# Optimization experiments

Measured on AMD Instinct MI355X. Metric: run time of the kernel, lower is better.

Reference implementation:

```python
import jax, jax.numpy as jnp
import numpy as np

N_NODES = 10000
N_EDGES = 320000
MUL = 32            # multiplicity of each irrep block (32x0e + 32x1o)
H = 4               # attention heads (divides MUL)
D_IN = MUL + 3 * MUL  # 128
N_BASIS = 8         # radial basis size (edge_scalar_attr dim)
HID = 64            # features=[64] hidden layer of the weight-MLP
INV3 = 1.0 / np.sqrt(3.0)  # CG normalization for 1o x 1o -> 0e


def _mlp(x, w1, b1, w2):
    # HTensorProductMLP weight net: edge scalars -> per-path uvu weights
    h = jax.nn.gelu(x @ w1 * (1.0 / np.sqrt(N_BASIS)) + b1)
    return (h @ w2) * (1.0 / np.sqrt(HID))  # (E, 4*MUL)


def _tp_uvu(w, xs, xv, ys, yv):
    # uvu tensor product of (32x0e+32x1o) x (1x0e+1x1o) keeping {0e,1o} outputs.
    # Sorted output blocks: [0e: s*s, 0e: v.v, 1o: s*v, 1o: v*s]
    w = w.reshape(-1, 4, MUL)
    o0 = w[:, 0] * xs * ys[:, None]                              # (E,MUL)
    o1 = w[:, 1] * jnp.einsum('eud,ed->eu', xv, yv) * INV3       # (E,MUL)
    o2 = w[:, 2][:, :, None] * xs[:, :, None] * yv[:, None, :]   # (E,MUL,3)
    o3 = w[:, 3][:, :, None] * xv * ys[:, None, None]            # (E,MUL,3)
    return o0, o1, o2, o3


def setup_inputs() -> dict:
    key = jax.random.key(0)
    ks = jax.random.split(key, 13)
    E, N = N_EDGES, N_NODES
    return {
        'edge_src': jax.random.randint(ks[0], (E,), 0, N, dtype=jnp.int32),
        'edge_dst': jax.random.randint(ks[1], (E,), 0, N, dtype=jnp.int32),
        'edge_scalar_attr': jax.random.uniform(ks[2], (E, N_BASIS), dtype=jnp.float32),
        'edge_attr': jax.random.normal(ks[3], (E, 4), dtype=jnp.float32),
        'edge_weight_cutoff': jax.random.uniform(ks[4], (E,), dtype=jnp.float32),
        'node_f': jax.random.normal(ks[5], (N, D_IN), dtype=jnp.float32),
        'wk1': jax.random.normal(ks[6], (N_BASIS, HID), dtype=jnp.float32),
        'bk1': jnp.zeros((HID,), jnp.float32),
        'wk2': jax.random.normal(ks[7], (HID, 4 * MUL), dtype=jnp.float32),
        'wv1': jax.random.normal(ks[8], (N_BASIS, HID), dtype=jnp.float32),
        'bv1': jnp.zeros((HID,), jnp.float32),
        'wv2': jax.random.normal(ks[9], (HID, 4 * MUL), dtype=jnp.float32),
        'W_dot': jax.random.normal(ks[10], (4, H, MUL, MUL), dtype=jnp.float32),
        'W_lin_s': jax.random.normal(ks[11], (2 * MUL, MUL), dtype=jnp.float32),
        'W_lin_v': jax.random.normal(ks[12], (2 * MUL, MUL), dtype=jnp.float32),
    }


def reference(edge_src, edge_dst, edge_scalar_attr, edge_attr, edge_weight_cutoff,
              node_f, wk1, bk1, wk2, wv1, bv1, wv2, W_dot, W_lin_s, W_lin_v):
    N = node_f.shape[0]
    xs = node_f[:, :MUL]                       # (N,MUL)   0e block
    xv = node_f[:, MUL:].reshape(N, MUL, 3)    # (N,MUL,3) 1o block
    ys = edge_attr[:, 0]                       # (E,)  Y_0
    yv = edge_attr[:, 1:4]                     # (E,3) Y_1
    sxs, sxv = xs[edge_src], xv[edge_src]      # gather source node feats

    # keys: per-edge equivariant tensor-product MLP
    wk = _mlp(edge_scalar_attr, wk1, bk1, wk2)
    k0, k1, kv0, kv1 = _tp_uvu(wk, sxs, sxv, ys, yv)

    # attention logits: fully-connected TP (dst node, key) -> Hx0e
    qs, qv = xs[edge_dst], xv[edge_dst]
    inv_fan = 1.0 / np.sqrt(4.0 * MUL * MUL)
    d = (jnp.einsum('huv,eu,ev->eh', W_dot[0], qs, k0)
         + jnp.einsum('huv,eu,ev->eh', W_dot[1], qs, k1)
         + jnp.einsum('huv,eud,evd->eh', W_dot[2], qv, kv0) * INV3
         + jnp.einsum('huv,eud,evd->eh', W_dot[3], qv, kv1) * INV3) * inv_fan
    expw = edge_weight_cutoff[:, None] * jnp.exp(d)              # (E,H)
    z = jax.ops.segment_sum(expw, edge_dst, num_segments=N)      # (N,H)
    z = jnp.where(z == 0.0, 1.0, z)
    alpha = expw / z[edge_dst]                                   # (E,H)

    # values: second per-edge equivariant tensor-product MLP
    wv = _mlp(edge_scalar_attr, wv1, bv1, wv2)
    v0, v1, vv0, vv1 = _tp_uvu(wv, sxs, sxv, ys, yv)
    sa = jnp.sqrt(jax.nn.relu(alpha))                            # (E,H)
    Ee = sa.shape[0]
    m = MUL // H
    e0 = (v0.reshape(Ee, H, m) * sa[:, :, None]).reshape(Ee, MUL)
    e1 = (v1.reshape(Ee, H, m) * sa[:, :, None]).reshape(Ee, MUL)
    e2 = (vv0.reshape(Ee, H, m, 3) * sa[:, :, None, None]).reshape(Ee, 3 * MUL)
    e3 = (vv1.reshape(Ee, H, m, 3) * sa[:, :, None, None]).reshape(Ee, 3 * MUL)
    edge_v = jnp.concatenate([e0, e1, e2, e3], axis=-1)          # (E, 8*MUL)

    agg = jax.ops.segment_sum(edge_v, edge_dst, num_segments=N)  # (N, 8*MUL)

    # equivariant HLinear: mix multiplicities within each irrep
    s = agg[:, :2 * MUL]                                         # (N,2*MUL)
    v = agg[:, 2 * MUL:].reshape(N, 2 * MUL, 3)                  # (N,2*MUL,3)
    inv_l = 1.0 / np.sqrt(2.0 * MUL)
    out_s = (s @ W_lin_s) * inv_l                                # (N,MUL)
    out_v = jnp.einsum('nud,uw->nwd', v, W_lin_v) * inv_l        # (N,MUL,3)
    return jnp.concatenate([out_s, out_v.reshape(N, 3 * MUL)], axis=-1)
```

## Files before the change

kernel.cpp:

```cpp
#include <hip/hip_runtime.h>


constexpr float INV3    = 0.57735026918962576f;
constexpr float INV_SQ8 = 0.35355339059327373f;
constexpr float INV_HID = 0.125f;
constexpr float INV_FAN = 0.015625f;
constexpr float INV_L   = 0.125f;
constexpr int   MAXD    = 128;

__device__ __forceinline__ float gelu_tanh(float x) {
  float u = 0.7978845608028654f * (x + 0.044715f * x * x * x);
  float e = __expf(2.0f * u);
  return x * (1.0f - 1.0f / (e + 1.0f));
}

__global__ void k_zero(int* __restrict__ p, int n) {
  int i = blockIdx.x * 256 + threadIdx.x;
  if (i < n) p[i] = 0;
}

__global__ void k_hist(const int* __restrict__ dst, int* __restrict__ cnt, int E) {
  int e = blockIdx.x * 256 + threadIdx.x;
  if (e < E) atomicAdd(&cnt[dst[e]], 1);
}

__global__ __launch_bounds__(256) void k_scan(const int* __restrict__ cnt,
                                              int* __restrict__ rowptr, int N) {
  __shared__ int wsum[4];
  __shared__ int woff[4];
  __shared__ int carry;
  int t = threadIdx.x, wave = t >> 6, lane = t & 63;
  if (t == 0) { carry = 0; rowptr[0] = 0; }
  __syncthreads();
  for (int base = 0; base < N; base += 256) {
    int i = base + t;
    int inc = (i < N) ? cnt[i] : 0;
#pragma unroll
    for (int off = 1; off < 64; off <<= 1) {
      int y = __shfl_up(inc, off, 64);
      if (lane >= off) inc += y;
    }
    if (lane == 63) wsum[wave] = inc;
    __syncthreads();
    if (t == 0) {
      int r = 0;
      for (int w = 0; w < 4; w++) { woff[w] = r; r += wsum[w]; }
    }
    __syncthreads();
    int incl = inc + woff[wave] + carry;
    if (i < N) rowptr[i + 1] = incl;
    __syncthreads();
    if (t == 255) carry = incl;
    __syncthreads();
  }
}

__global__ void k_fill(const int* __restrict__ dst, const int* __restrict__ rowptr,
                       int* __restrict__ cursor, int* __restrict__ csr, int E) {
  int e = blockIdx.x * 256 + threadIdx.x;
  if (e < E) {
    int d = dst[e];
    int s = atomicAdd(&cursor[d], 1);
    csr[rowptr[d] + s] = e;
  }
}

__global__ void k_dhist(const int* __restrict__ rowptr, int* __restrict__ dbin, int N) {
  int n = blockIdx.x * 256 + threadIdx.x;
  if (n < N) {
    int deg = rowptr[n + 1] - rowptr[n];
    atomicAdd(&dbin[min(deg, 127)], 1);
  }
}

__global__ void k_dscan(const int* __restrict__ dbin, int* __restrict__ doff) {
  if (threadIdx.x == 0 && blockIdx.x == 0) {
    int r = 0;
    for (int d = 127; d >= 0; --d) { doff[d] = r; r += dbin[d]; }
  }
}

__global__ void k_dfill(const int* __restrict__ rowptr, const int* __restrict__ doff,
                        int* __restrict__ dcur, int* __restrict__ nperm, int N) {
  int n = blockIdx.x * 256 + threadIdx.x;
  if (n < N) {
    int d = min(rowptr[n + 1] - rowptr[n], 127);
    int p = doff[d] + atomicAdd(&dcur[d], 1);
    nperm[p] = n;
  }
}

__global__ __launch_bounds__(256) void k_gather(
    const int* __restrict__ csr, const int* __restrict__ esrc,
    const float* __restrict__ xattr, const float* __restrict__ eattr,
    const float* __restrict__ cutoff,
    float* __restrict__ xc, float* __restrict__ ec, float* __restrict__ cc,
    int* __restrict__ srcc, int E) {
  int p = blockIdx.x * 256 + threadIdx.x;
  if (p >= E) return;
  int e = csr[p];
  srcc[p] = esrc[e];
  cc[p] = cutoff[e];
  ((float4*)ec)[p] = ((const float4*)eattr)[e];
  const float4* xs = (const float4*)xattr + (size_t)e * 2;
  float4* xd = (float4*)xc + (size_t)p * 2;
  xd[0] = xs[0]; xd[1] = xs[1];
}

__global__ __launch_bounds__(256) void k_nodeA(const float* __restrict__ node_f,
                                               const float* __restrict__ Wdot,
                                               float* __restrict__ A, int N) {
  __shared__ float Wd[16384];
  __shared__ float nfs[32 * 128];
  int t = threadIdx.x;
  for (int i = t; i < 16384; i += 256) Wd[i] = Wdot[i];
  int n0 = blockIdx.x * 32;
  int nEnd = min(32, N - n0);
  for (int i = t; i < nEnd * 128; i += 256) nfs[i] = node_f[n0 * 128 + i];
  __syncthreads();
  for (int nn = 0; nn < nEnd; ++nn) {
    const float* nf = &nfs[nn * 128];
    float* An = &A[(n0 + nn) * 1024];
#pragma unroll
    for (int k = 0; k < 4; k++) {
      int o = t + k * 256;
      float acc = 0.f;
      int idx;
      if (o < 256) {
        int term = o >> 7, h = (o >> 5) & 3, v = o & 31;
        const float* W = &Wd[term * 4096 + h * 1024 + v];
#pragma unroll
        for (int u = 0; u < 32; u++) acc += W[u * 32] * nf[u];
        idx = term * 128 + v * 4 + h;
      } else {
        int r = o - 256;
        int term = r / 384;
        int rr = r % 384;
        int h = rr / 96, q = rr % 96, v = q / 3, d = q - 3 * (q / 3);
        const float* W = &Wd[(term + 2) * 4096 + h * 1024 + v];
#pragma unroll
        for (int u = 0; u < 32; u++) acc += W[u * 32] * nf[32 + u * 3 + d];
        idx = 256 + term * 384 + v * 12 + h * 3 + d;
      }
      An[idx] = acc;
    }
  }
}

__global__ __launch_bounds__(256) void k_mlp(
    const float* __restrict__ xc,
    const float* __restrict__ w1, const float* __restrict__ b1,
    const float* __restrict__ w2,
    float* __restrict__ wm,
    int E, int chunk)
{
  __shared__ __align__(16) float w1s[512];
  __shared__ float b1s[64];
  __shared__ __align__(16) float wq[16][128][4];
  __shared__ __align__(16) float Hs[4][4][64];

  int t = threadIdx.x;
  int wave = t >> 6, lane = t & 63;
  for (int i = t; i < 512; i += 256) w1s[i] = w1[i];
  if (t < 64) b1s[t] = b1[t];
  for (int i = t; i < 8192; i += 256) { int l = i >> 7, j = i & 127; wq[l >> 2][j][l & 3] = w2[i]; }
  __syncthreads();

  int base = blockIdx.x * chunk;
  int end = min(base + chunk, E);
  int v = lane & 31;
  bool hi = lane >= 32;

  for (int sb = base + wave * 4; sb < end; sb += 16) {
    int sl[4];
#pragma unroll
    for (int k = 0; k < 4; k++) sl[k] = min(sb + k, E - 1);
    float h[4];
#pragma unroll
    for (int k = 0; k < 4; k++) {
      const float4* xp = (const float4*)xc + (size_t)sl[k] * 2;
      float4 xa = xp[0], xb = xp[1];
      float acc = xa.x * w1s[lane]       + xa.y * w1s[64 + lane]
                + xa.z * w1s[128 + lane] + xa.w * w1s[192 + lane]
                + xb.x * w1s[256 + lane] + xb.y * w1s[320 + lane]
                + xb.z * w1s[384 + lane] + xb.w * w1s[448 + lane];
      h[k] = gelu_tanh(acc * INV_SQ8 + b1s[lane]);
    }
#pragma unroll
    for (int k = 0; k < 4; k++) Hs[wave][k][lane] = h[k];
    float a0[4] = {0, 0, 0, 0}, a1[4] = {0, 0, 0, 0};
#pragma unroll
    for (int q = 0; q < 16; q++) {
      float4 wA = *(const float4*)&wq[q][lane][0];
      float4 wB = *(const float4*)&wq[q][lane + 64][0];
#pragma unroll
      for (int k = 0; k < 4; k++) {
        float4 hq = *(const float4*)&Hs[wave][k][q * 4];
        a0[k] += hq.x * wA.x + hq.y * wA.y + hq.z * wA.z + hq.w * wA.w;
        a1[k] += hq.x * wB.x + hq.y * wB.y + hq.z * wB.z + hq.w * wB.w;
      }
    }
#pragma unroll
    for (int k = 0; k < 4; k++) {
      if (sb + k < end) {
        float2 o = make_float2(a0[k] * INV_HID, a1[k] * INV_HID);
        ((float2*)wm)[(size_t)sl[k] * 64 + (hi ? 32 : 0) + v] = o;
      }
    }
  }
}

__global__ __launch_bounds__(256) void k_att(
    const int* __restrict__ rowptr,
    const int* __restrict__ nperm,
    const int* __restrict__ srcc,
    const float* __restrict__ ec,
    const float* __restrict__ cc,
    const float* __restrict__ node_f,
    const float* __restrict__ wm,
    const float* __restrict__ A,
    float* __restrict__ sa_out,
    int N)
{
  __shared__ float expws[4][MAXD][4];

  int t = threadIdx.x;
  int wave = t >> 6, lane = t & 63;
  int idx = blockIdx.x * 4 + wave;
  if (idx >= N) return;
  int n = nperm[idx];
  int row0 = rowptr[n];
  int deg = min(rowptr[n + 1] - row0, MAXD);
  if (deg <= 0) return;

  int v = lane & 31;
  bool hi = lane >= 32;
  int kk = (lane >> 2) & 3;

  float aS[4], aV[12];
  {
    const float* Ab = A + (size_t)n * 1024;
    const float* ps = Ab + (hi ? 128 : 0) + v * 4;
    float4 t0 = *(const float4*)ps;
    aS[0] = t0.x; aS[1] = t0.y; aS[2] = t0.z; aS[3] = t0.w;
    const float* pv = Ab + (hi ? 640 : 256) + v * 12;
    float4 u0 = *(const float4*)pv;
    float4 u1 = *(const float4*)(pv + 4);
    float4 u2 = *(const float4*)(pv + 8);
    aV[0] = u0.x; aV[1] = u0.y; aV[2]  = u0.z; aV[3]  = u0.w;
    aV[4] = u1.x; aV[5] = u1.y; aV[6]  = u1.z; aV[7]  = u1.w;
    aV[8] = u2.x; aV[9] = u2.y; aV[10] = u2.z; aV[11] = u2.w;
  }

  int iters = (deg + 3) >> 2;
  float zacc = 0.f;

  for (int it = 0; it < iters; ++it) {
    int sb = it * 4;
    int slot[4]; int sp[4];
#pragma unroll
    for (int k = 0; k < 4; k++) slot[k] = row0 + min(sb + k, deg - 1);
#pragma unroll
    for (int k = 0; k < 4; k++) sp[k] = srcc[slot[k]];
    float4 ya[4]; float cf[4]; float2 wj[4]; float s0[4], s1[4], s2[4];
#pragma unroll
    for (int k = 0; k < 4; k++) {
      ya[k] = ((const float4*)ec)[slot[k]];
      cf[k] = (sb + k < deg) ? cc[slot[k]] : 0.f;
      wj[k] = ((const float2*)wm)[(size_t)slot[k] * 64 + (hi ? 32 : 0) + v];
      const float* nf = &node_f[(size_t)sp[k] * 128];
      if (!hi) { s0[k] = nf[v]; s1[k] = 0.f; s2[k] = 0.f; }
      else     { s0[k] = nf[32 + v * 3]; s1[k] = nf[33 + v * 3]; s2[k] = nf[34 + v * 3]; }
    }
    float p[16];
#pragma unroll
    for (int k = 0; k < 4; k++) {
      float ys = ya[k].x, yv0 = ya[k].y, yv1 = ya[k].z, yv2 = ya[k].w;
      if (!hi) {
        float k0 = wj[k].x * s0[k] * ys;
        float kb = INV3 * wj[k].y * s0[k];
#pragma unroll
        for (int h2 = 0; h2 < 4; h2++)
          p[k * 4 + h2] = aS[h2] * k0 +
              kb * (aV[h2 * 3] * yv0 + aV[h2 * 3 + 1] * yv1 + aV[h2 * 3 + 2] * yv2);
      } else {
        float dotv = s0[k] * yv0 + s1[k] * yv1 + s2[k] * yv2;
        float k1 = wj[k].x * dotv * INV3;
        float kc = INV3 * wj[k].y * ys;
#pragma unroll
        for (int h2 = 0; h2 < 4; h2++)
          p[k * 4 + h2] = aS[h2] * k1 +
              kc * (aV[h2 * 3] * s0[k] + aV[h2 * 3 + 1] * s1[k] + aV[h2 * 3 + 2] * s2[k]);
      }
    }
    bool fb0 = (lane & 1) != 0;
    float q8[8];
#pragma unroll
    for (int j = 0; j < 8; j++) {
      float a = p[2 * j], b = p[2 * j + 1];
      float keep = fb0 ? b : a, send = fb0 ? a : b;
      q8[j] = keep + __shfl_xor(send, 1, 64);
    }
    bool fb1 = (lane & 2) != 0;
    float r4[4];
#pragma unroll
    for (int j = 0; j < 4; j++) {
      float a = q8[2 * j], b = q8[2 * j + 1];
      float keep = fb1 ? b : a, send = fb1 ? a : b;
      r4[j] = keep + __shfl_xor(send, 2, 64);
    }
    bool fb2 = (lane & 4) != 0;
    float s2v[2];
#pragma unroll
    for (int j = 0; j < 2; j++) {
      float a = r4[2 * j], b = r4[2 * j + 1];
      float keep = fb2 ? b : a, send = fb2 ? a : b;
      s2v[j] = keep + __shfl_xor(send, 4, 64);
    }
    bool fb3 = (lane & 8) != 0;
    float w;
    {
      float a = s2v[0], b = s2v[1];
      float keep = fb3 ? b : a, send = fb3 ? a : b;
      w = keep + __shfl_xor(send, 8, 64);
    }
    w += __shfl_xor(w, 16, 64);
    w += __shfl_xor(w, 32, 64);
    float cA = (lane & 4) ? cf[1] : cf[0];
    float cB = (lane & 4) ? cf[3] : cf[2];
    float cfs = (lane & 8) ? cB : cA;
    int slotw = sb + kk;
    float ex = cfs * __expf(w * INV_FAN);
    if (lane < 16 && slotw < deg) {
      expws[wave][slotw][lane & 3] = ex;
      zacc += ex;
    }
  }
  float zr = zacc;
  zr += __shfl_xor(zr, 4, 64);
  zr += __shfl_xor(zr, 8, 64);
  float zf = __shfl(zr, lane & 3, 64);
  zf = (zf == 0.f) ? 1.f : zf;
  for (int i = lane; i < deg * 4; i += 64) {
    int slot = i >> 2;
    float alpha = expws[wave][slot][lane & 3] / zf;
    sa_out[(size_t)(row0 + slot) * 4 + (lane & 3)] = sqrtf(fmaxf(alpha, 0.f));
  }
}

__global__ __launch_bounds__(256) void k_agg(
    const int* __restrict__ rowptr,
    const int* __restrict__ nperm,
    const int* __restrict__ srcc,
    const float* __restrict__ ec,
    const float* __restrict__ node_f,
    const float* __restrict__ wm,
    const float* __restrict__ Wls, const float* __restrict__ Wlv,
    const float* __restrict__ sa_in,
    float* __restrict__ out,
    int N)
{
  __shared__ float aggv[4][256];

  int t = threadIdx.x;
  int wave = t >> 6, lane = t & 63;
  int idx = blockIdx.x * 4 + wave;
  if (idx >= N) return;
  int n = nperm[idx];
  int row0 = rowptr[n];
  int deg = min(rowptr[n + 1] - row0, MAXD);

  int v = lane & 31;
  bool hi = lane >= 32;
  int hh = v >> 3;
  float accS = 0.f, acc0 = 0.f, acc1 = 0.f, acc2 = 0.f;

  if (deg > 0) {
    int iters = (deg + 3) >> 2;
    for (int it = 0; it < iters; ++it) {
      int sb = it * 4;
      int slot[4]; int sp[4];
#pragma unroll
      for (int k = 0; k < 4; k++) slot[k] = row0 + min(sb + k, deg - 1);
#pragma unroll
      for (int k = 0; k < 4; k++) sp[k] = srcc[slot[k]];
      float4 ya[4]; float sav[4]; float2 wj[4]; float s0[4], s1[4], s2[4];
#pragma unroll
      for (int k = 0; k < 4; k++) {
        sav[k] = (sb + k < deg) ? sa_in[(size_t)slot[k] * 4 + hh] : 0.f;
        ya[k] = ((const float4*)ec)[slot[k]];
        wj[k] = ((const float2*)wm)[(size_t)slot[k] * 64 + (hi ? 32 : 0) + v];
        const float* nf = &node_f[(size_t)sp[k] * 128];
        if (!hi) { s0[k] = nf[v]; s1[k] = 0.f; s2[k] = 0.f; }
        else     { s0[k] = nf[32 + v * 3]; s1[k] = nf[33 + v * 3]; s2[k] = nf[34 + v * 3]; }
      }
#pragma unroll
      for (int k = 0; k < 4; k++) {
        float ys = ya[k].x, yv0 = ya[k].y, yv1 = ya[k].z, yv2 = ya[k].w;
        float sav_k = sav[k];
        if (!hi) {
          accS += wj[k].x * s0[k] * ys * sav_k;
          float b = wj[k].y * s0[k] * sav_k;
          acc0 += b * yv0; acc1 += b * yv1; acc2 += b * yv2;
        } else {
          float dotv = s0[k] * yv0 + s1[k] * yv1 + s2[k] * yv2;
          accS += wj[k].x * dotv * INV3 * sav_k;
          float c = wj[k].y * ys * sav_k;
          acc0 += c * s0[k]; acc1 += c * s1[k]; acc2 += c * s2[k];
        }
      }
    }
  }
  {
    int us = hi ? 32 + v : v;
    aggv[wave][us]       = accS;
    aggv[wave][64 + us]  = acc0;
    aggv[wave][128 + us] = acc1;
    aggv[wave][192 + us] = acc2;
    const float* agg = aggv[wave];
#pragma unroll
    for (int rep = 0; rep < 2; ++rep) {
      int o = lane + rep * 64;
      float acc = 0.f;
      if (o < 32) {
#pragma unroll
        for (int u = 0; u < 64; u++) acc += agg[u] * Wls[u * 32 + o];
      } else {
        int i = o - 32, w2 = i / 3, d = i - 3 * w2;
        const float* av = &agg[64 + d * 64];
#pragma unroll
        for (int u = 0; u < 64; u++) acc += av[u] * Wlv[u * 32 + w2];
      }
      out[(size_t)n * 128 + o] = acc * INV_L;
    }
  }
}

extern "C" void kernel_launch(void* const* d_in, const int* in_sizes, int n_in,
                              void* d_out, int out_size, void* d_ws, size_t ws_size,
                              hipStream_t stream) {
  const int*   esrc   = (const int*)d_in[0];
  const int*   edst   = (const int*)d_in[1];
  const float* xattr  = (const float*)d_in[2];
  const float* eattr  = (const float*)d_in[3];
  const float* cutoff = (const float*)d_in[4];
  const float* node_f = (const float*)d_in[5];
  const float* wk1    = (const float*)d_in[6];
  const float* bk1    = (const float*)d_in[7];
  const float* wk2    = (const float*)d_in[8];
  const float* wv1    = (const float*)d_in[9];
  const float* bv1    = (const float*)d_in[10];
  const float* wv2    = (const float*)d_in[11];
  const float* Wdot   = (const float*)d_in[12];
  const float* Wls    = (const float*)d_in[13];
  const float* Wlv    = (const float*)d_in[14];
  float* out = (float*)d_out;

  int E = in_sizes[0];
  int N = in_sizes[5] / 128;

  float* A    = (float*)d_ws;
  float* sa   = A + (size_t)N * 1024;
  float* xc   = sa + (size_t)E * 4;
  float* ec   = xc + (size_t)E * 8;
  float* cc   = ec + (size_t)E * 4;
  int* srcc   = (int*)(cc + (size_t)E);
  int* counts = srcc + E;
  int* cursor = counts + N;
  int* dbin   = cursor + N;
  int* dcur   = dbin + 128;
  int* rowptr = dcur + 128;
  int* doff   = rowptr + (N + 1);
  int* nperm  = doff + 128;
  int* csr    = nperm + N;
  float* wm   = (float*)(csr + E);

  k_zero<<<(2 * N + 256 + 255) / 256, 256, 0, stream>>>(counts, 2 * N + 256);
  k_hist<<<(E + 255) / 256, 256, 0, stream>>>(edst, counts, E);
  k_scan<<<1, 256, 0, stream>>>(counts, rowptr, N);
  k_fill<<<(E + 255) / 256, 256, 0, stream>>>(edst, rowptr, cursor, csr, E);
  k_dhist<<<(N + 255) / 256, 256, 0, stream>>>(rowptr, dbin, N);
  k_dscan<<<1, 64, 0, stream>>>(dbin, doff);
  k_dfill<<<(N + 255) / 256, 256, 0, stream>>>(rowptr, doff, dcur, nperm, N);
  k_gather<<<(E + 255) / 256, 256, 0, stream>>>(csr, esrc, xattr, eattr, cutoff,
                                                xc, ec, cc, srcc, E);
  k_nodeA<<<(N + 31) / 32, 256, 0, stream>>>(node_f, Wdot, A, N);

  int chunk = 512;
  int mgrid = (E + chunk - 1) / chunk;
  int nb = (N + 3) / 4;

  k_mlp<<<mgrid, 256, 0, stream>>>(xc, wk1, bk1, wk2, wm, E, chunk);
  k_att<<<nb, 256, 0, stream>>>(rowptr, nperm, srcc, ec, cc, node_f, wm, A, sa, N);
  k_mlp<<<mgrid, 256, 0, stream>>>(xc, wv1, bv1, wv2, wm, E, chunk);
  k_agg<<<nb, 256, 0, stream>>>(rowptr, nperm, srcc, ec, node_f, wm,
                                Wls, Wlv, sa, out, N);
}
```

Before: 952.3 us.

## Restructure weight-MLP to one edge per thread with register-held hidden layer

The MLP kernel now assigns one edge per lane, keeps all 64 hidden activations in registers, and reads w1/w2 directly from global memory as wave-uniform (scalar) loads instead of staging them in shared memory. The grid becomes a fixed-size grid-stride loop. This is meant to remove the LDS traffic and the per-block weight staging. The trade-offs are heavy register pressure from h[64] plus the accumulators, which may cause spills or low occupancy, and output stores that are strided per lane and poorly coalesced.

Result: slower. 1.331 ms (+39.7%).

```diff
diff --git a/kernel.cpp b/kernel.cpp
--- a/kernel.cpp
+++ b/kernel.cpp
@@ -149,62 +149,51 @@
 
 __global__ __launch_bounds__(256) void k_mlp(
     const float* __restrict__ xc,
-    const float* __restrict__ w1, const float* __restrict__ b1,
+    const float* __restrict__ w1,
+    const float* __restrict__ b1,
     const float* __restrict__ w2,
     float* __restrict__ wm,
-    int E, int chunk)
+    int E)
 {
-  __shared__ __align__(16) float w1s[512];
-  __shared__ float b1s[64];
-  __shared__ __align__(16) float wq[16][128][4];
-  __shared__ __align__(16) float Hs[4][4][64];
-
-  int t = threadIdx.x;
-  int wave = t >> 6, lane = t & 63;
-  for (int i = t; i < 512; i += 256) w1s[i] = w1[i];
-  if (t < 64) b1s[t] = b1[t];
-  for (int i = t; i < 8192; i += 256) { int l = i >> 7, j = i & 127; wq[l >> 2][j][l & 3] = w2[i]; }
-  __syncthreads();
-
-  int base = blockIdx.x * chunk;
-  int end = min(base + chunk, E);
-  int v = lane & 31;
-  bool hi = lane >= 32;
-
-  for (int sb = base + wave * 4; sb < end; sb += 16) {
-    int sl[4];
-#pragma unroll
-    for (int k = 0; k < 4; k++) sl[k] = min(sb + k, E - 1);
-    float h[4];
-#pragma unroll
-    for (int k = 0; k < 4; k++) {
-      const float4* xp = (const float4*)xc + (size_t)sl[k] * 2;
-      float4 xa = xp[0], xb = xp[1];
-      float acc = xa.x * w1s[lane]       + xa.y * w1s[64 + lane]
-                + xa.z * w1s[128 + lane] + xa.w * w1s[192 + lane]
-                + xb.x * w1s[256 + lane] + xb.y * w1s[320 + lane]
-                + xb.z * w1s[384 + lane] + xb.w * w1s[448 + lane];
-      h[k] = gelu_tanh(acc * INV_SQ8 + b1s[lane]);
-    }
-#pragma unroll
-    for (int k = 0; k < 4; k++) Hs[wave][k][lane] = h[k];
-    float a0[4] = {0, 0, 0, 0}, a1[4] = {0, 0, 0, 0};
-#pragma unroll
-    for (int q = 0; q < 16; q++) {
-      float4 wA = *(const float4*)&wq[q][lane][0];
-      float4 wB = *(const float4*)&wq[q][lane + 64][0];
-#pragma unroll
-      for (int k = 0; k < 4; k++) {
-        float4 hq = *(const float4*)&Hs[wave][k][q * 4];
-        a0[k] += hq.x * wA.x + hq.y * wA.y + hq.z * wA.z + hq.w * wA.w;
-        a1[k] += hq.x * wB.x + hq.y * wB.y + hq.z * wB.z + hq.w * wB.w;
-      }
-    }
-#pragma unroll
-    for (int k = 0; k < 4; k++) {
-      if (sb + k < end) {
-        float2 o = make_float2(a0[k] * INV_HID, a1[k] * INV_HID);
-        ((float2*)wm)[(size_t)sl[k] * 64 + (hi ? 32 : 0) + v] = o;
+  int lane = threadIdx.x & 63;
+  int wave = threadIdx.x >> 6;
+  int stride = gridDim.x * 256;
+
+  for (int eb = blockIdx.x * 256 + wave * 64; eb < E; eb += stride) {
+    int slot = min(eb + lane, E - 1);
+    bool valid = (eb + lane) < E;
+    const float4* xp = (const float4*)xc + (size_t)slot * 2;
+    float4 xa = xp[0], xb = xp[1];
+    float h[64];
+#pragma unroll
+    for (int l = 0; l < 64; ++l) {
+      float acc = xa.x * w1[l]       + xa.y * w1[64 + l]
+                + xa.z * w1[128 + l] + xa.w * w1[192 + l]
+                + xb.x * w1[256 + l] + xb.y * w1[320 + l]
+                + xb.z * w1[384 + l] + xb.w * w1[448 + l];
+      h[l] = gelu_tanh(acc * INV_SQ8 + b1[l]);
+    }
+    float2* wrow = (float2*)wm + (size_t)slot * 64;
+    for (int jc = 0; jc < 8; ++jc) {
+      float a0[8] = {0, 0, 0, 0, 0, 0, 0, 0};
+      float a1[8] = {0, 0, 0, 0, 0, 0, 0, 0};
+      const float* wj = w2 + jc * 8;
+#pragma unroll
+      for (int l = 0; l < 64; ++l) {
+        const float* wr = wj + l * 128;
+#pragma unroll
+        for (int j = 0; j < 8; ++j) {
+          a0[j] += h[l] * wr[j];
+          a1[j] += h[l] * wr[64 + j];
+        }
+      }
+      if (valid) {
+        float4* wp = (float4*)(wrow + jc * 8);
+#pragma unroll
+        for (int j = 0; j < 4; ++j) {
+          wp[j] = make_float4(a0[2 * j] * INV_HID,     a1[2 * j] * INV_HID,
+                              a0[2 * j + 1] * INV_HID, a1[2 * j + 1] * INV_HID);
+        }
       }
     }
   }
@@ -486,13 +475,12 @@
                                                 xc, ec, cc, srcc, E);
   k_nodeA<<<(N + 31) / 32, 256, 0, stream>>>(node_f, Wdot, A, N);
 
-  int chunk = 512;
-  int mgrid = (E + chunk - 1) / chunk;
+  int mgrid = 640;
   int nb = (N + 3) / 4;
 
-  k_mlp<<<mgrid, 256, 0, stream>>>(xc, wk1, bk1, wk2, wm, E, chunk);
+  k_mlp<<<mgrid, 256, 0, stream>>>(xc, wk1, bk1, wk2, wm, E);
   k_att<<<nb, 256, 0, stream>>>(rowptr, nperm, srcc, ec, cc, node_f, wm, A, sa, N);
-  k_mlp<<<mgrid, 256, 0, stream>>>(xc, wv1, bv1, wv2, wm, E, chunk);
+  k_mlp<<<mgrid, 256, 0, stream>>>(xc, wv1, bv1, wv2, wm, E);
   k_agg<<<nb, 256, 0, stream>>>(rowptr, nperm, srcc, ec, node_f, wm,
                                 Wls, Wlv, sa, out, N);
 }
```

## Restructure weight-MLP second layer to share hidden rows across waves

Applied to the files above, without the earlier changes.

The second MLP layer now stages 16 edges' hidden activations in a block-shared, padded tile. Each thread owns one output column pair and computes it for 4 edges, reading float2 weights from a padded shared array instead of float4 quads over 128 outputs. The grid is also fixed to 512 blocks, with the per-block chunk derived from E and rounded to 16. This cuts per-thread weight traffic and improves reuse, but adds two block-wide barriers per 16-edge step. A local variable in the attention kernel is renamed.

Result: slower. 1.006 ms (+5.7%).

```diff
diff --git a/kernel.cpp b/kernel.cpp
--- a/kernel.cpp
+++ b/kernel.cpp
@@ -149,62 +149,69 @@
 
 __global__ __launch_bounds__(256) void k_mlp(
     const float* __restrict__ xc,
-    const float* __restrict__ w1, const float* __restrict__ b1,
+    const float* __restrict__ w1,
+    const float* __restrict__ b1,
     const float* __restrict__ w2,
     float* __restrict__ wm,
     int E, int chunk)
 {
   __shared__ __align__(16) float w1s[512];
   __shared__ float b1s[64];
-  __shared__ __align__(16) float wq[16][128][4];
-  __shared__ __align__(16) float Hs[4][4][64];
+  __shared__ __align__(16) float2 wqs[64][65];
+  __shared__ __align__(16) float Hs[16][68];
 
   int t = threadIdx.x;
   int wave = t >> 6, lane = t & 63;
   for (int i = t; i < 512; i += 256) w1s[i] = w1[i];
   if (t < 64) b1s[t] = b1[t];
-  for (int i = t; i < 8192; i += 256) { int l = i >> 7, j = i & 127; wq[l >> 2][j][l & 3] = w2[i]; }
+  for (int i = t; i < 4096; i += 256) {
+    int l = i >> 6, p = i & 63;
+    wqs[p][l] = make_float2(w2[l * 128 + p], w2[l * 128 + 64 + p]);
+  }
   __syncthreads();
 
   int base = blockIdx.x * chunk;
   int end = min(base + chunk, E);
-  int v = lane & 31;
-  bool hi = lane >= 32;
-
-  for (int sb = base + wave * 4; sb < end; sb += 16) {
-    int sl[4];
-#pragma unroll
-    for (int k = 0; k < 4; k++) sl[k] = min(sb + k, E - 1);
-    float h[4];
-#pragma unroll
-    for (int k = 0; k < 4; k++) {
-      const float4* xp = (const float4*)xc + (size_t)sl[k] * 2;
+  int p    = (wave << 4) + (lane & 15);
+  int esub = lane >> 4;
+
+  for (int sb = base; sb < end; sb += 16) {
+    float hv[4];
+#pragma unroll
+    for (int s = 0; s < 4; ++s) {
+      int slot = min(sb + wave + 4 * s, E - 1);
+      const float4* xp = (const float4*)xc + (size_t)slot * 2;
       float4 xa = xp[0], xb = xp[1];
       float acc = xa.x * w1s[lane]       + xa.y * w1s[64 + lane]
                 + xa.z * w1s[128 + lane] + xa.w * w1s[192 + lane]
                 + xb.x * w1s[256 + lane] + xb.y * w1s[320 + lane]
                 + xb.z * w1s[384 + lane] + xb.w * w1s[448 + lane];
-      h[k] = gelu_tanh(acc * INV_SQ8 + b1s[lane]);
-    }
-#pragma unroll
-    for (int k = 0; k < 4; k++) Hs[wave][k][lane] = h[k];
+      hv[s] = gelu_tanh(acc * INV_SQ8 + b1s[lane]);
+    }
+    __syncthreads();
+#pragma unroll
+    for (int s = 0; s < 4; ++s) Hs[wave + 4 * s][lane] = hv[s];
+    __syncthreads();
     float a0[4] = {0, 0, 0, 0}, a1[4] = {0, 0, 0, 0};
-#pragma unroll
-    for (int q = 0; q < 16; q++) {
-      float4 wA = *(const float4*)&wq[q][lane][0];
-      float4 wB = *(const float4*)&wq[q][lane + 64][0];
-#pragma unroll
-      for (int k = 0; k < 4; k++) {
-        float4 hq = *(const float4*)&Hs[wave][k][q * 4];
-        a0[k] += hq.x * wA.x + hq.y * wA.y + hq.z * wA.z + hq.w * wA.w;
-        a1[k] += hq.x * wB.x + hq.y * wB.y + hq.z * wB.z + hq.w * wB.w;
-      }
-    }
-#pragma unroll
-    for (int k = 0; k < 4; k++) {
-      if (sb + k < end) {
-        float2 o = make_float2(a0[k] * INV_HID, a1[k] * INV_HID);
-        ((float2*)wm)[(size_t)sl[k] * 64 + (hi ? 32 : 0) + v] = o;
+    for (int lb = 0; lb < 16; ++lb) {
+      float2 wl0 = wqs[p][lb * 4 + 0];
+      float2 wl1 = wqs[p][lb * 4 + 1];
+      float2 wl2 = wqs[p][lb * 4 + 2];
+      float2 wl3 = wqs[p][lb * 4 + 3];
+#pragma unroll
+      for (int s = 0; s < 4; ++s) {
+        int e = esub * 4 + s;
+        float4 hq = *(const float4*)&Hs[e][lb * 4];
+        a0[s] += hq.x * wl0.x + hq.y * wl1.x + hq.z * wl2.x + hq.w * wl3.x;
+        a1[s] += hq.x * wl0.y + hq.y * wl1.y + hq.z * wl2.y + hq.w * wl3.y;
+      }
+    }
+#pragma unroll
+    for (int s = 0; s < 4; ++s) {
+      int slot = sb + esub * 4 + s;
+      if (slot < end) {
+        ((float2*)wm)[(size_t)slot * 64 + p] =
+            make_float2(a0[s] * INV_HID, a1[s] * INV_HID);
       }
     }
   }
@@ -272,7 +279,7 @@
       if (!hi) { s0[k] = nf[v]; s1[k] = 0.f; s2[k] = 0.f; }
       else     { s0[k] = nf[32 + v * 3]; s1[k] = nf[33 + v * 3]; s2[k] = nf[34 + v * 3]; }
     }
-    float p[16];
+    float p4[16];
 #pragma unroll
     for (int k = 0; k < 4; k++) {
       float ys = ya[k].x, yv0 = ya[k].y, yv1 = ya[k].z, yv2 = ya[k].w;
@@ -281,7 +288,7 @@
         float kb = INV3 * wj[k].y * s0[k];
 #pragma unroll
         for (int h2 = 0; h2 < 4; h2++)
-          p[k * 4 + h2] = aS[h2] * k0 +
+          p4[k * 4 + h2] = aS[h2] * k0 +
               kb * (aV[h2 * 3] * yv0 + aV[h2 * 3 + 1] * yv1 + aV[h2 * 3 + 2] * yv2);
       } else {
         float dotv = s0[k] * yv0 + s1[k] * yv1 + s2[k] * yv2;
@@ -289,7 +296,7 @@
         float kc = INV3 * wj[k].y * ys;
 #pragma unroll
         for (int h2 = 0; h2 < 4; h2++)
-          p[k * 4 + h2] = aS[h2] * k1 +
+          p4[k * 4 + h2] = aS[h2] * k1 +
               kc * (aV[h2 * 3] * s0[k] + aV[h2 * 3 + 1] * s1[k] + aV[h2 * 3 + 2] * s2[k]);
       }
     }
@@ -297,7 +304,7 @@
     float q8[8];
 #pragma unroll
     for (int j = 0; j < 8; j++) {
-      float a = p[2 * j], b = p[2 * j + 1];
+      float a = p4[2 * j], b = p4[2 * j + 1];
       float keep = fb0 ? b : a, send = fb0 ? a : b;
       q8[j] = keep + __shfl_xor(send, 1, 64);
     }
@@ -486,8 +493,8 @@
                                                 xc, ec, cc, srcc, E);
   k_nodeA<<<(N + 31) / 32, 256, 0, stream>>>(node_f, Wdot, A, N);
 
-  int chunk = 512;
-  int mgrid = (E + chunk - 1) / chunk;
+  int mgrid = 512;
+  int chunk = ((E + mgrid - 1) / mgrid + 15) & ~15;
   int nb = (N + 3) / 4;
 
   k_mlp<<<mgrid, 256, 0, stream>>>(xc, wk1, bk1, wk2, wm, E, chunk);
```
